# Optimization experiments

Hardware: AMD Instinct MI355X
Metric: run time of the kernel (lower is better)

## Reference

```python
import jax, jax.numpy as jnp
import numpy as np

B, N, C = 8, 1024, 1024
H = 16
D = C // H  # head_dim = 64
SCALE = D ** -0.5


def setup_inputs() -> dict:
    key = jax.random.key(0)
    k1, k2, k3, k4 = jax.random.split(key, 4)
    x = jax.random.normal(k1, (B, N, C), dtype=jnp.float32)
    qkv_w = jax.random.normal(k2, (3 * C, C), dtype=jnp.float32) * (C ** -0.5)
    proj_w = jax.random.normal(k3, (C, C), dtype=jnp.float32) * (C ** -0.5)
    proj_b = jax.random.normal(k4, (C,), dtype=jnp.float32)
    return {"x": x, "qkv_w": qkv_w, "proj_w": proj_w, "proj_b": proj_b}


def reference(x, qkv_w, proj_w, proj_b):
    # qkv projection: torch Linear weight is [out, in] -> x @ W^T
    qkv = jnp.einsum('bnc,oc->bno', x, qkv_w)            # [B, N, 3C]
    qkv = qkv.reshape(B, N, 3, H, D)
    q = jnp.transpose(qkv[:, :, 0], (0, 2, 1, 3))        # [B, H, N, D]
    k = jnp.transpose(qkv[:, :, 1], (0, 2, 1, 3))
    v = jnp.transpose(qkv[:, :, 2], (0, 2, 1, 3))
    attn = jnp.einsum('bhqd,bhkd->bhqk', q, k) * SCALE   # [B, H, N, N]
    attn = jax.nn.softmax(attn, axis=-1)
    out = jnp.einsum('bhqk,bhkd->bhqd', attn, v)         # [B, H, N, D]
    out = jnp.transpose(out, (0, 2, 1, 3)).reshape(B, N, C)
    out = jnp.einsum('bnc,oc->bno', out, proj_w) + proj_b
    return out
```

## Files before the change

kernel.cpp:

```cpp
#include <hip/hip_runtime.h>
#include <hip/hip_bf16.h>
#include <stdint.h>

#define B_ 8
#define N_ 1024
#define C_ 1024
#define H_ 16

static constexpr float SCALE = 0.125f;
static constexpr float LOG2E = 1.4426950408889634f;
static constexpr float SL    = SCALE * LOG2E;

typedef __attribute__((ext_vector_type(4))) float f32x4;
typedef __attribute__((ext_vector_type(8))) short s16x8;

__device__ __forceinline__ ushort f2bf(float f) {
    union { float f; uint32_t u; } c; c.f = f;
    uint32_t u = c.u;
    return (ushort)((u + 0x7fffu + ((u >> 16) & 1u)) >> 16);
}

__device__ __forceinline__ ushort f2bfc(float f) {
    union { __hip_bfloat16 h; ushort u; } c;
    c.h = __float2bfloat16(f);
    return c.u;
}

__device__ __forceinline__ void gload_lds16(const void* g, void* l) {
    __builtin_amdgcn_global_load_lds(
        (const __attribute__((address_space(1))) void*)g,
        (__attribute__((address_space(3))) void*)l,
        16, 0, 0);
}
__device__ __forceinline__ void gload_lds4(const void* g, void* l) {
    __builtin_amdgcn_global_load_lds(
        (const __attribute__((address_space(1))) void*)g,
        (__attribute__((address_space(3))) void*)l,
        4, 0, 0);
}

__global__ __launch_bounds__(256) void cvt_f32_bf16(const float* __restrict__ in,
                                                    ushort* __restrict__ out, int n4) {
    int i = blockIdx.x * 256 + threadIdx.x;
    if (i >= n4) return;
    float4 v = ((const float4*)in)[i];
    ushort4 o = make_ushort4(f2bf(v.x), f2bf(v.y), f2bf(v.z), f2bf(v.w));
    ((ushort4*)out)[i] = o;
}

__global__ __launch_bounds__(256) void cvt_qkvw(const float* __restrict__ in,
                                                ushort* __restrict__ out, int n4) {
    int i = blockIdx.x * 256 + threadIdx.x;
    if (i >= n4) return;
    float4 v = ((const float4*)in)[i];
    const float sc = (i < (1024 * 1024 / 4)) ? SL : 1.0f;
    ushort4 o = make_ushort4(f2bf(v.x * sc), f2bf(v.y * sc), f2bf(v.z * sc), f2bf(v.w * sc));
    ((ushort4*)out)[i] = o;
}

template<int OUT_BF16>
__global__ __launch_bounds__(256) void gemm_bt(const ushort* __restrict__ A,
                                               const ushort* __restrict__ Bw,
                                               void* __restrict__ Cout,
                                               const float* __restrict__ bias,
                                               int M, int Nout, int K) {
    __shared__ ushort Asm[128 * 64];
    __shared__ ushort Bsm[128 * 64];
    const int t = threadIdx.x;
    const int l = t & 63, w = t >> 6;
    const int lq = l & 15, lg = l >> 4;
    const int trow = blockIdx.y * 128, tcol = blockIdx.x * 128;
    const int wrow = (w >> 1) * 64, wcol = (w & 1) * 64;

    f32x4 acc[4][4] = {};

    const int srow0 = t >> 3;
    const int sc8 = (((t & 7) ^ (srow0 & 7)) * 8);
    const size_t abase = (size_t)(trow + srow0) * K + sc8;
    const size_t bbase = (size_t)(tcol + srow0) * K + sc8;

    for (int k0 = 0; k0 < K; k0 += 64) {
#pragma unroll
        for (int i = 0; i < 4; ++i) {
            gload_lds16(A + abase + (size_t)i * 32 * K + k0, &Asm[(i * 256 + w * 64) * 8]);
            gload_lds16(Bw + bbase + (size_t)i * 32 * K + k0, &Bsm[(i * 256 + w * 64) * 8]);
        }
        __syncthreads();
#pragma unroll
        for (int kk = 0; kk < 2; ++kk) {
            s16x8 af[4], bf[4];
#pragma unroll
            for (int m = 0; m < 4; ++m) {
                int row = wrow + m * 16 + lq;
                int ch = (kk * 4 + lg) ^ (row & 7);
                af[m] = *(const s16x8*)&Asm[row * 64 + ch * 8];
            }
#pragma unroll
            for (int n = 0; n < 4; ++n) {
                int row = wcol + n * 16 + lq;
                int ch = (kk * 4 + lg) ^ (row & 7);
                bf[n] = *(const s16x8*)&Bsm[row * 64 + ch * 8];
            }
#pragma unroll
            for (int m = 0; m < 4; ++m)
#pragma unroll
                for (int n = 0; n < 4; ++n)
                    acc[m][n] = __builtin_amdgcn_mfma_f32_16x16x32_bf16(af[m], bf[n], acc[m][n], 0, 0, 0);
        }
        __syncthreads();
    }

#pragma unroll
    for (int m = 0; m < 4; ++m)
#pragma unroll
        for (int n = 0; n < 4; ++n)
#pragma unroll
            for (int r = 0; r < 4; ++r) {
                int row = trow + wrow + m * 16 + lg * 4 + r;
                int col = tcol + wcol + n * 16 + lq;
                if (OUT_BF16) {
                    ((ushort*)Cout)[(size_t)row * Nout + col] = f2bfc(acc[m][n][r]);
                } else {
                    ((float*)Cout)[(size_t)row * Nout + col] = acc[m][n][r] + bias[col];
                }
            }
}

__global__ __launch_bounds__(512, 2) void gemm_bt256(const ushort* __restrict__ A,
                                                     const ushort* __restrict__ Bw,
                                                     ushort* __restrict__ Cout,
                                                     int M, int Nout, int K) {
    __shared__ ushort Asm[2][256 * 64];
    __shared__ ushort Bsm[2][256 * 64];
    const int t = threadIdx.x;
    const int l = t & 63, w = t >> 6;
    const int lq = l & 15, lg = l >> 4;
    const int wm = w >> 2, wn = w & 3;

    int bid = blockIdx.y * gridDim.x + blockIdx.x;
    const int cpx = (gridDim.x * gridDim.y) >> 3;
    bid = (bid & 7) * cpx + (bid >> 3);
    const int bx = bid % gridDim.x, by = bid / gridDim.x;
    const int trow = by * 256, tcol = bx * 256;

    f32x4 acc[8][4] = {};

    const int srow = t >> 3;
    const int scc = ((t & 7) ^ (srow & 7)) * 8;
    const size_t abase = (size_t)(trow + srow) * K + scc;
    const size_t bbase = (size_t)(tcol + srow) * K + scc;

#define STAGE256(buf, k0)                                                      \
    {                                                                          \
        _Pragma("unroll")                                                      \
        for (int j = 0; j < 4; ++j) {                                          \
            gload_lds16(A + abase + (size_t)j * 64 * K + (k0),                 \
                        &Asm[buf][(j * 512 + t) * 8]);                         \
            gload_lds16(Bw + bbase + (size_t)j * 64 * K + (k0),                \
                        &Bsm[buf][(j * 512 + t) * 8]);                         \
        }                                                                      \
    }
#define LOAD_A256(qr)                                                          \
    _Pragma("unroll") for (int m = 0; m < 4; ++m) {                            \
        const int row = wm * 128 + (qr) * 64 + m * 16 + lq;                    \
        _Pragma("unroll") for (int kk = 0; kk < 2; ++kk)                       \
            af[m][kk] = *(const s16x8*)&Asm[cur][row * 64 +                    \
                            (((kk * 4 + lg) ^ (row & 7)) * 8)];                \
    }
#define LOAD_B256(qc)                                                          \
    _Pragma("unroll") for (int n = 0; n < 2; ++n) {                            \
        const int row = wn * 64 + (qc) * 32 + n * 16 + lq;                     \
        _Pragma("unroll") for (int kk = 0; kk < 2; ++kk)                       \
            bf[n][kk] = *(const s16x8*)&Bsm[cur][row * 64 +                    \
                            (((kk * 4 + lg) ^ (row & 7)) * 8)];                \
    }
#define MFMA_Q256(qr, qc)                                                      \
    __builtin_amdgcn_s_setprio(1);                                             \
    _Pragma("unroll") for (int m = 0; m < 4; ++m)                              \
        _Pragma("unroll") for (int n = 0; n < 2; ++n)                          \
            _Pragma("unroll") for (int kk = 0; kk < 2; ++kk)                   \
                acc[(qr) * 4 + m][(qc) * 2 + n] =                              \
                    __builtin_amdgcn_mfma_f32_16x16x32_bf16(                   \
                        af[m][kk], bf[n][kk], acc[(qr) * 4 + m][(qc) * 2 + n], \
                        0, 0, 0);                                              \
    __builtin_amdgcn_s_setprio(0);

    STAGE256(0, 0);
    asm volatile("s_waitcnt vmcnt(0)" ::: "memory");
    __builtin_amdgcn_s_barrier();

    const int NT = K / 64;
    for (int kt = 0; kt < NT; ++kt) {
        const int cur = kt & 1, nxt = cur ^ 1;
        s16x8 af[4][2], bf[2][2];
        LOAD_A256(0); LOAD_B256(0);
        if (kt < NT - 1) STAGE256(nxt, (kt + 1) * 64);
        __builtin_amdgcn_s_barrier();
        MFMA_Q256(0, 0);
        __builtin_amdgcn_s_barrier();
        LOAD_B256(1);
        __builtin_amdgcn_s_barrier();
        MFMA_Q256(0, 1);
        __builtin_amdgcn_s_barrier();
        LOAD_A256(1);
        __builtin_amdgcn_s_barrier();
        MFMA_Q256(1, 1);
        __builtin_amdgcn_s_barrier();
        LOAD_B256(0);
        __builtin_amdgcn_s_barrier();
        MFMA_Q256(1, 0);
        asm volatile("s_waitcnt vmcnt(0)" ::: "memory");
        __builtin_amdgcn_s_barrier();
    }

#pragma unroll
    for (int mt = 0; mt < 8; ++mt)
#pragma unroll
        for (int nt = 0; nt < 4; ++nt)
#pragma unroll
            for (int r = 0; r < 4; ++r) {
                int row = trow + wm * 128 + mt * 16 + lg * 4 + r;
                int col = tcol + wn * 64 + nt * 16 + lq;
                Cout[(size_t)row * Nout + col] = f2bfc(acc[mt][nt][r]);
            }
#undef STAGE256
#undef LOAD_A256
#undef LOAD_B256
#undef MFMA_Q256
}

__global__ __launch_bounds__(256) void attn_fwd(const ushort* __restrict__ qk,
                                                const ushort* __restrict__ vt,
                                                ushort* __restrict__ attn_out) {
    __shared__ ushort Klds[64 * 64];
    __shared__ ushort Vlds[64 * 64];

    const int t = threadIdx.x, l = t & 63, w = t >> 6;
    const int lq = l & 15, lg = l >> 4;

    const int serial = blockIdx.x + 16 * blockIdx.y;
    const int logical = (serial & 7) * 256 + (serial >> 3);
    const int qt = logical & 15;
    const int bh = logical >> 4;
    const int b = bh >> 4, h = bh & 15;

    const int qrow = qt * 64 + w * 16 + lq;
    const size_t qoff = (size_t)(b * N_ + qrow) * 2048 + h * 64;
    const s16x8 qf0 = *(const s16x8*)&qk[qoff + lg * 8];
    const s16x8 qf1 = *(const s16x8*)&qk[qoff + 32 + lg * 8];

    float l_run = 0.f;
    f32x4 o[4] = {};

    const int srow0 = t >> 3;
    const int sc8 = ((t & 7) ^ (srow0 & 7)) * 8;
    const size_t kgbase = (size_t)(b * N_ + srow0) * 2048 + 1024 + h * 64 + sc8;

    const ushort* vptr[8];
#pragma unroll
    for (int j = 0; j < 8; ++j) {
        const int d = 16 * w + 2 * j + (l >> 5);
        const int c = ((l & 31) >> 2) ^ (d & 7);
        const int s = c * 8 + (l & 3) * 2;
        const int key = (s >> 5) * 32 + ((s >> 2) & 1) * 16 + ((s >> 3) & 3) * 4 + (s & 3);
        vptr[j] = vt + (size_t)(h * 64 + d) * (B_ * N_) + b * N_ + key;
    }

    for (int kt = 0; kt < N_ / 64; ++kt) {
        const size_t koff = kgbase + (size_t)kt * 64 * 2048;
        gload_lds16(qk + koff, &Klds[w * 512]);
        gload_lds16(qk + koff + (size_t)32 * 2048, &Klds[2048 + w * 512]);
#pragma unroll
        for (int j = 0; j < 8; ++j)
            gload_lds4(vptr[j] + kt * 64, &Vlds[w * 1024 + j * 128]);
        __syncthreads();

        f32x4 s[4];
#pragma unroll
        for (int g = 0; g < 4; ++g) {
            int key = g * 16 + lq;
            const s16x8 kf0 = *(const s16x8*)&Klds[key * 64 + ((lg ^ (key & 7)) * 8)];
            const s16x8 kf1 = *(const s16x8*)&Klds[key * 64 + (((4 + lg) ^ (key & 7)) * 8)];
            f32x4 z = {};
            z    = __builtin_amdgcn_mfma_f32_16x16x32_bf16(kf0, qf0, z, 0, 0, 0);
            s[g] = __builtin_amdgcn_mfma_f32_16x16x32_bf16(kf1, qf1, z, 0, 0, 0);
        }

        float pv[4][4];
        float psum = 0.f;
#pragma unroll
        for (int g = 0; g < 4; ++g) {
            float p0 = __builtin_amdgcn_exp2f(s[g][0]);
            float p1 = __builtin_amdgcn_exp2f(s[g][1]);
            float p2 = __builtin_amdgcn_exp2f(s[g][2]);
            float p3 = __builtin_amdgcn_exp2f(s[g][3]);
            psum += (p0 + p1) + (p2 + p3);
            pv[g][0] = p0; pv[g][1] = p1; pv[g][2] = p2; pv[g][3] = p3;
        }
        l_run += psum;

#pragma unroll
        for (int kb = 0; kb < 2; ++kb) {
            s16x8 pfrag;
#pragma unroll
            for (int i = 0; i < 4; ++i) {
                pfrag[i]     = (short)f2bfc(pv[2 * kb][i]);
                pfrag[4 + i] = (short)f2bfc(pv[2 * kb + 1][i]);
            }
#pragma unroll
            for (int ds = 0; ds < 4; ++ds) {
                const s16x8 vf = *(const s16x8*)
                    &Vlds[(ds * 16 + lq) * 64 + (((kb * 4 + lg) ^ (lq & 7)) * 8)];
                o[ds] = __builtin_amdgcn_mfma_f32_16x16x32_bf16(pfrag, vf, o[ds], 0, 0, 0);
            }
        }
        __syncthreads();
    }

    l_run += __shfl_xor(l_run, 16);
    l_run += __shfl_xor(l_run, 32);

#pragma unroll
    for (int r = 0; r < 4; ++r) {
        float rl = 1.f / __shfl(l_run, lg * 4 + r);
        int orow = qt * 64 + w * 16 + lg * 4 + r;
        size_t base = (size_t)(b * N_ + orow) * C_ + h * 64 + lq;
#pragma unroll
        for (int ds = 0; ds < 4; ++ds)
            attn_out[base + ds * 16] = f2bfc(o[ds][r] * rl);
    }
}

extern "C" void kernel_launch(void* const* d_in, const int* in_sizes, int n_in,
                              void* d_out, int out_size, void* d_ws, size_t ws_size,
                              hipStream_t stream) {
    const float* x      = (const float*)d_in[0];
    const float* qkv_w  = (const float*)d_in[1];
    const float* proj_w = (const float*)d_in[2];
    const float* proj_b = (const float*)d_in[3];
    float* out = (float*)d_out;

    ushort* ws    = (ushort*)d_ws;
    ushort* xb    = ws;
    ushort* wqkv  = xb + (size_t)8192 * 1024;
    ushort* wproj = wqkv + (size_t)3072 * 1024;
    ushort* qkb   = wproj + (size_t)1024 * 1024;
    ushort* vtb   = qkb + (size_t)8192 * 2048;
    ushort* attn  = vtb + (size_t)1024 * 8192;

    cvt_f32_bf16<<<8192, 256, 0, stream>>>(x, xb, 2097152);
    cvt_qkvw<<<3072, 256, 0, stream>>>(qkv_w, wqkv, 786432);
    cvt_f32_bf16<<<1024, 256, 0, stream>>>(proj_w, wproj, 262144);

    gemm_bt256<<<dim3(8, 32), 512, 0, stream>>>(xb, wqkv, qkb, 8192, 2048, 1024);
    gemm_bt<1><<<dim3(64, 8), 256, 0, stream>>>(wqkv + (size_t)2048 * 1024, xb, (void*)vtb,
                                                nullptr, 1024, 8192, 1024);

    attn_fwd<<<dim3(16, 128), 256, 0, stream>>>(qkb, vtb, attn);

    gemm_bt<0><<<dim3(8, 64), 256, 0, stream>>>(attn, wproj, (void*)out, proj_b, 8192, 1024, 1024);
}
```

Baseline: 163.6 us.

## Merge conversion kernels and widen attention blocks to 128 query rows

The three fp32-to-bf16 conversion launches become one kernel that routes each index range to its source and destination, which removes launch overhead. The attention kernel now runs 512 threads (8 waves) per block covering 128 query rows instead of 64. Each K/V tile loaded into LDS is therefore shared by twice as many waves, and K/V global traffic is halved. The trade-off is fewer blocks, larger blocks and lower occupancy flexibility.

```diff
diff --git a/kernel.cpp b/kernel.cpp
--- a/kernel.cpp
+++ b/kernel.cpp
@@ -39,23 +39,29 @@
         4, 0, 0);
 }
 
-__global__ __launch_bounds__(256) void cvt_f32_bf16(const float* __restrict__ in,
-                                                    ushort* __restrict__ out, int n4) {
+__global__ __launch_bounds__(256) void cvt_all(const float* __restrict__ x,
+                                               const float* __restrict__ qkv_w,
+                                               const float* __restrict__ proj_w,
+                                               ushort* __restrict__ xb,
+                                               ushort* __restrict__ wqkv,
+                                               ushort* __restrict__ wproj) {
     int i = blockIdx.x * 256 + threadIdx.x;
-    if (i >= n4) return;
-    float4 v = ((const float4*)in)[i];
-    ushort4 o = make_ushort4(f2bf(v.x), f2bf(v.y), f2bf(v.z), f2bf(v.w));
-    ((ushort4*)out)[i] = o;
-}
-
-__global__ __launch_bounds__(256) void cvt_qkvw(const float* __restrict__ in,
-                                                ushort* __restrict__ out, int n4) {
-    int i = blockIdx.x * 256 + threadIdx.x;
-    if (i >= n4) return;
-    float4 v = ((const float4*)in)[i];
-    const float sc = (i < (1024 * 1024 / 4)) ? SL : 1.0f;
+    const float* src;
+    ushort* dst;
+    float sc = 1.0f;
+    if (i < 2097152) {
+        src = x; dst = xb;
+    } else if (i < 2097152 + 786432) {
+        i -= 2097152;
+        src = qkv_w; dst = wqkv;
+        if (i < 262144) sc = SL;
+    } else {
+        i -= 2097152 + 786432;
+        src = proj_w; dst = wproj;
+    }
+    float4 v = ((const float4*)src)[i];
     ushort4 o = make_ushort4(f2bf(v.x * sc), f2bf(v.y * sc), f2bf(v.z * sc), f2bf(v.w * sc));
-    ((ushort4*)out)[i] = o;
+    ((ushort4*)dst)[i] = o;
 }
 
 template<int OUT_BF16>
@@ -229,7 +235,7 @@
 #undef MFMA_Q256
 }
 
-__global__ __launch_bounds__(256) void attn_fwd(const ushort* __restrict__ qk,
+__global__ __launch_bounds__(512) void attn_fwd(const ushort* __restrict__ qk,
                                                 const ushort* __restrict__ vt,
                                                 ushort* __restrict__ attn_out) {
     __shared__ ushort Klds[64 * 64];
@@ -238,13 +244,13 @@
     const int t = threadIdx.x, l = t & 63, w = t >> 6;
     const int lq = l & 15, lg = l >> 4;
 
-    const int serial = blockIdx.x + 16 * blockIdx.y;
-    const int logical = (serial & 7) * 256 + (serial >> 3);
-    const int qt = logical & 15;
-    const int bh = logical >> 4;
+    const int serial = blockIdx.x + 8 * blockIdx.y;
+    const int logical = (serial & 7) * 128 + (serial >> 3);
+    const int qt = logical & 7;
+    const int bh = logical >> 3;
     const int b = bh >> 4, h = bh & 15;
 
-    const int qrow = qt * 64 + w * 16 + lq;
+    const int qrow = qt * 128 + w * 16 + lq;
     const size_t qoff = (size_t)(b * N_ + qrow) * 2048 + h * 64;
     const s16x8 qf0 = *(const s16x8*)&qk[qoff + lg * 8];
     const s16x8 qf1 = *(const s16x8*)&qk[qoff + 32 + lg * 8];
@@ -256,10 +262,10 @@
     const int sc8 = ((t & 7) ^ (srow0 & 7)) * 8;
     const size_t kgbase = (size_t)(b * N_ + srow0) * 2048 + 1024 + h * 64 + sc8;
 
-    const ushort* vptr[8];
-#pragma unroll
-    for (int j = 0; j < 8; ++j) {
-        const int d = 16 * w + 2 * j + (l >> 5);
+    const ushort* vptr[4];
+#pragma unroll
+    for (int j = 0; j < 4; ++j) {
+        const int d = 8 * w + 2 * j + (l >> 5);
         const int c = ((l & 31) >> 2) ^ (d & 7);
         const int s = c * 8 + (l & 3) * 2;
         const int key = (s >> 5) * 32 + ((s >> 2) & 1) * 16 + ((s >> 3) & 3) * 4 + (s & 3);
@@ -267,12 +273,10 @@
     }
 
     for (int kt = 0; kt < N_ / 64; ++kt) {
-        const size_t koff = kgbase + (size_t)kt * 64 * 2048;
-        gload_lds16(qk + koff, &Klds[w * 512]);
-        gload_lds16(qk + koff + (size_t)32 * 2048, &Klds[2048 + w * 512]);
-#pragma unroll
-        for (int j = 0; j < 8; ++j)
-            gload_lds4(vptr[j] + kt * 64, &Vlds[w * 1024 + j * 128]);
+        gload_lds16(qk + kgbase + (size_t)kt * 64 * 2048, &Klds[w * 512]);
+#pragma unroll
+        for (int j = 0; j < 4; ++j)
+            gload_lds4(vptr[j] + kt * 64, &Vlds[w * 512 + j * 128]);
         __syncthreads();
 
         f32x4 s[4];
@@ -323,7 +327,7 @@
 #pragma unroll
     for (int r = 0; r < 4; ++r) {
         float rl = 1.f / __shfl(l_run, lg * 4 + r);
-        int orow = qt * 64 + w * 16 + lg * 4 + r;
+        int orow = qt * 128 + w * 16 + lg * 4 + r;
         size_t base = (size_t)(b * N_ + orow) * C_ + h * 64 + lq;
 #pragma unroll
         for (int ds = 0; ds < 4; ++ds)
@@ -348,15 +352,13 @@
     ushort* vtb   = qkb + (size_t)8192 * 2048;
     ushort* attn  = vtb + (size_t)1024 * 8192;
 
-    cvt_f32_bf16<<<8192, 256, 0, stream>>>(x, xb, 2097152);
-    cvt_qkvw<<<3072, 256, 0, stream>>>(qkv_w, wqkv, 786432);
-    cvt_f32_bf16<<<1024, 256, 0, stream>>>(proj_w, wproj, 262144);
+    cvt_all<<<12288, 256, 0, stream>>>(x, qkv_w, proj_w, xb, wqkv, wproj);
 
     gemm_bt256<<<dim3(8, 32), 512, 0, stream>>>(xb, wqkv, qkb, 8192, 2048, 1024);
     gemm_bt<1><<<dim3(64, 8), 256, 0, stream>>>(wqkv + (size_t)2048 * 1024, xb, (void*)vtb,
                                                 nullptr, 1024, 8192, 1024);
 
-    attn_fwd<<<dim3(16, 128), 256, 0, stream>>>(qkb, vtb, attn);
+    attn_fwd<<<dim3(8, 128), 512, 0, stream>>>(qkb, vtb, attn);
 
     gemm_bt<0><<<dim3(8, 64), 256, 0, stream>>>(attn, wproj, (void*)out, proj_b, 8192, 1024, 1024);
 }
```

Measured after the change: 154.5 us. -5.6%, faster.
